# Performance work log

Hardware: AMD Instinct MI355X
Metric: run time of the kernel (lower is better)

Reference implementation:

```python
import jax, jax.numpy as jnp
import numpy as np

N_NODES = 50000
N_EDGES = 800000
N_REL = 2
K_SEL = 4096


def _glorot(key, shape):
    fan = shape[-2] + shape[-1]
    lim = jnp.sqrt(6.0 / fan)
    return jax.random.uniform(key, shape, minval=-lim, maxval=lim, dtype=jnp.float32)


def setup_inputs() -> dict:
    key = jax.random.key(0)
    ks = jax.random.split(key, 12)
    x = jax.random.normal(ks[0], (N_NODES, 128), jnp.float32)
    edge_index = jax.random.randint(ks[1], (2, N_EDGES), 0, N_NODES)
    edge_type = jax.random.randint(ks[2], (N_EDGES,), 0, N_REL)
    idx = jax.random.randint(ks[3], (K_SEL,), 0, N_NODES)
    # RGATConv 0: in=128, out=128, heads=2, dim=1 -> concat width 256
    w0 = _glorot(ks[4], (N_REL, 128, 256))
    q0 = _glorot(ks[5], (256, 2))
    k0 = _glorot(ks[6], (256, 2))
    b0 = jnp.zeros((256,), jnp.float32)
    g0 = jnp.ones((256,), jnp.float32)
    be0 = jnp.zeros((256,), jnp.float32)
    # RGATConv 1: in=256, out=128, heads=1
    w1 = _glorot(ks[7], (N_REL, 256, 128))
    q1 = _glorot(ks[8], (128, 1))
    k1 = _glorot(ks[9], (128, 1))
    b1 = jnp.zeros((128,), jnp.float32)
    g1 = jnp.ones((128,), jnp.float32)
    be1 = jnp.zeros((128,), jnp.float32)
    wm = _glorot(ks[10], (128, 5))
    bm = jnp.zeros((5,), jnp.float32)
    return dict(x=x, edge_index=edge_index, edge_type=edge_type, idx=idx,
                w0=w0, q0=q0, k0=k0, b0=b0, g0=g0, be0=be0,
                w1=w1, q1=q1, k1=k1, b1=b1, g1=g1, be1=be1, wm=wm, bm=bm)


def _segment_softmax(a, index, num_segments):
    # PyG utils.softmax: per-target max-shifted exp, normalized with +1e-16
    m = jax.ops.segment_max(a, index, num_segments=num_segments)
    m = jnp.where(jnp.isfinite(m), m, 0.0)
    e = jnp.exp(a - m[index])
    s = jax.ops.segment_sum(e, index, num_segments=num_segments)
    return e / (s[index] + 1e-16)


def _rgat(x, W, q, k, b, src, dst, edge_type, heads, out_ch, n):
    # additive-self-attention, across-relation, dim=1, aggr='add' (PyG defaults)
    xw = jnp.einsum('ni,rio->rno', x, W)          # [R, N, H*O]
    out_i = xw[edge_type, dst]                    # [E, H*O] gathered per edge
    out_j = xw[edge_type, src]                    # [E, H*O]
    alpha = jax.nn.leaky_relu(out_i @ q + out_j @ k, 0.2)   # [E, H]
    alpha = _segment_softmax(alpha, dst, n)
    msg = (alpha[:, :, None] * out_j.reshape(-1, heads, out_ch)).reshape(-1, heads * out_ch)
    return jax.ops.segment_sum(msg, dst, num_segments=n) + b


def _bn(h, g, b):
    # training-mode BatchNorm over nodes (biased var, eps=1e-5)
    mu = jnp.mean(h, axis=0)
    var = jnp.var(h, axis=0)
    return g * (h - mu) * jax.lax.rsqrt(var + 1e-5) + b


def reference(x, edge_index, edge_type, idx, w0, q0, k0, b0, g0, be0,
              w1, q1, k1, b1, g1, be1, wm, bm):
    n = x.shape[0]
    src, dst = edge_index[0], edge_index[1]
    h = jax.nn.leaky_relu(_rgat(x, w0, q0, k0, b0, src, dst, edge_type, 2, 128, n), 0.01)
    h = _bn(h, g0, be0)
    h = jax.nn.leaky_relu(_rgat(h, w1, q1, k1, b1, src, dst, edge_type, 1, 128, n), 0.01)
    h = _bn(h, g1, be1)
    h = h[idx]                                   # index_select over nodes
    out = jax.nn.sigmoid(h @ wm + bm)
    return (h, out)
```

## Files before the change

kernel.cpp:

```cpp
#include <hip/hip_runtime.h>
#include <hip/hip_bf16.h>
#include <math.h>


#define WAVE 64

typedef short     s16x8 __attribute__((ext_vector_type(8)));
typedef float     f32x4 __attribute__((ext_vector_type(4)));
typedef _Float16  f16x8 __attribute__((ext_vector_type(8)));
typedef _Float16  f16x4 __attribute__((ext_vector_type(4)));
typedef _Float16  f16x2 __attribute__((ext_vector_type(2)));

__device__ inline ushort bf_rne(float x) {
  uint u = __float_as_uint(x);
  return (ushort)((u + 0x7FFFu + ((u >> 16) & 1u)) >> 16);
}
__device__ inline ushort bf_hi_resid(float x, float& resid) {
  uint u = __float_as_uint(x);
  uint r = (u + 0x7FFFu + ((u >> 16) & 1u)) & 0xFFFF0000u;
  resid = x - __uint_as_float(r);
  return (ushort)(r >> 16);
}

__global__ __launch_bounds__(256) void k_hist(const int* __restrict__ dst,
                                              int* __restrict__ deg, int E) {
  int e = blockIdx.x * blockDim.x + threadIdx.x;
  if (e < E) atomicAdd(&deg[dst[e]], 1);
}

__global__ __launch_bounds__(256) void k_scan_blk(const int* __restrict__ deg,
                                                  int* __restrict__ bsum, int n) {
  int i = blockIdx.x * 256 + threadIdx.x;
  int v = (i < n) ? deg[i] : 0;
#pragma unroll
  for (int o = 32; o; o >>= 1) v += __shfl_xor(v, o);
  __shared__ int ws[4];
  if ((threadIdx.x & 63) == 0) ws[threadIdx.x >> 6] = v;
  __syncthreads();
  if (threadIdx.x == 0) bsum[blockIdx.x] = ws[0] + ws[1] + ws[2] + ws[3];
}

__global__ __launch_bounds__(256) void k_scan_top(int* __restrict__ bsum, int nb,
                                                  int* __restrict__ rowptr_n,
                                                  int E) {
  __shared__ int sh[256];
  int t = threadIdx.x;
  int carry = 0;
  for (int base = 0; base < nb; base += 256) {
    int i = base + t;
    int v = (i < nb) ? bsum[i] : 0;
    sh[t] = v;
    __syncthreads();
    for (int o = 1; o < 256; o <<= 1) {
      int u = (t >= o) ? sh[t - o] : 0;
      __syncthreads();
      sh[t] += u;
      __syncthreads();
    }
    if (i < nb) bsum[i] = carry + sh[t] - v;
    int blockTotal = sh[255];
    __syncthreads();
    carry += blockTotal;
  }
  if (t == 0) *rowptr_n = E;
}

__global__ __launch_bounds__(256) void k_scan_fin(const int* __restrict__ deg,
                                                  const int* __restrict__ bsum,
                                                  int* __restrict__ rowptr,
                                                  int* __restrict__ cursor, int n) {
  int t = threadIdx.x;
  int i = blockIdx.x * 256 + t;
  int v = (i < n) ? deg[i] : 0;
  __shared__ int sh[256];
  sh[t] = v;
  __syncthreads();
  for (int o = 1; o < 256; o <<= 1) {
    int u = (t >= o) ? sh[t - o] : 0;
    __syncthreads();
    sh[t] += u;
    __syncthreads();
  }
  if (i < n) {
    int ex = bsum[blockIdx.x] + sh[t] - v;
    rowptr[i] = ex;
    cursor[i] = ex;
  }
}

__global__ __launch_bounds__(256) void k_scatter(const int* __restrict__ dst,
                                                 int* __restrict__ cursor,
                                                 int* __restrict__ csr, int E) {
  int e = blockIdx.x * blockDim.x + threadIdx.x;
  if (e < E) {
    int p = atomicAdd(&cursor[dst[e]], 1);
    csr[p] = e;
  }
}

__global__ __launch_bounds__(256) void k_split(const float* __restrict__ in,
                                               ushort* __restrict__ hi,
                                               ushort* __restrict__ lo,
                                               const float* __restrict__ scale,
                                               const float* __restrict__ shift,
                                               int n4, int Cmask) {
  int i = blockIdx.x * blockDim.x + threadIdx.x;
  if (i >= n4) return;
  float4 v = ((const float4*)in)[i];
  if (scale) {
    int c = (i * 4) & Cmask;
    v.x = v.x * scale[c + 0] + shift[c + 0];
    v.y = v.y * scale[c + 1] + shift[c + 1];
    v.z = v.z * scale[c + 2] + shift[c + 2];
    v.w = v.w * scale[c + 3] + shift[c + 3];
  }
  float r0, r1, r2, r3;
  ushort4 hv, lv;
  hv.x = bf_hi_resid(v.x, r0); lv.x = bf_rne(r0);
  hv.y = bf_hi_resid(v.y, r1); lv.y = bf_rne(r1);
  hv.z = bf_hi_resid(v.z, r2); lv.z = bf_rne(r2);
  hv.w = bf_hi_resid(v.w, r3); lv.w = bf_rne(r3);
  ((ushort4*)hi)[i] = hv;
  ((ushort4*)lo)[i] = lv;
}

__global__ __launch_bounds__(256) void k_convW(const float* __restrict__ w,
                                               ushort* __restrict__ thi,
                                               ushort* __restrict__ tlo,
                                               int R, int K, int N) {
  int i = blockIdx.x * blockDim.x + threadIdx.x;
  if (i >= R * K * N) return;
  int n  = i % N;
  int t  = i / N;
  int kk = t % K;
  int r  = t / K;
  float x = w[i];
  float resid;
  ushort h = bf_hi_resid(x, resid);
  size_t o = ((size_t)r * N + n) * K + kk;
  thi[o] = h;
  tlo[o] = bf_rne(resid);
}

__global__ __launch_bounds__(256) void k_gemm_mfma(
    const ushort* __restrict__ Ahi, const ushort* __restrict__ Alo,
    const ushort* __restrict__ Bhi, const ushort* __restrict__ Blo,
    _Float16* __restrict__ C, int M, int K, int N) {
  const int r  = blockIdx.z;
  const int n0 = blockIdx.x * 128;
  const int m0 = blockIdx.y * 128;
  __shared__ __align__(16) ushort Ah[128][40];
  __shared__ __align__(16) ushort Al[128][40];
  __shared__ __align__(16) ushort Bh[128][40];
  __shared__ __align__(16) ushort Bl[128][40];
  const int tid  = threadIdx.x;
  const int lane = tid & 63;
  const int wid  = tid >> 6;
  const int wr = wid >> 1, wc = wid & 1;
  const int lr = lane & 15;
  const int lk = (lane >> 4) * 8;
  const size_t bbase = (size_t)r * N * K;

  f32x4 acc[4][4];
#pragma unroll
  for (int i = 0; i < 4; ++i)
#pragma unroll
    for (int j = 0; j < 4; ++j) acc[i][j] = (f32x4){0.f, 0.f, 0.f, 0.f};

  for (int k0 = 0; k0 < K; k0 += 32) {
#pragma unroll
    for (int rep = 0; rep < 2; ++rep) {
      int idx = tid + rep * 256;
      int row = idx >> 2, piece = idx & 3;
      int gm = m0 + row;
      s16x8 vh = (s16x8)0, vl = (s16x8)0;
      if (gm < M) {
        size_t ga = (size_t)gm * K + k0 + piece * 8;
        vh = *(const s16x8*)(Ahi + ga);
        vl = *(const s16x8*)(Alo + ga);
      }
      *(s16x8*)&Ah[row][piece * 8] = vh;
      *(s16x8*)&Al[row][piece * 8] = vl;
    }
#pragma unroll
    for (int rep = 0; rep < 2; ++rep) {
      int idx = tid + rep * 256;
      int col = idx >> 2, piece = idx & 3;
      size_t ga = bbase + (size_t)(n0 + col) * K + k0 + piece * 8;
      *(s16x8*)&Bh[col][piece * 8] = *(const s16x8*)(Bhi + ga);
      *(s16x8*)&Bl[col][piece * 8] = *(const s16x8*)(Blo + ga);
    }
    __syncthreads();

    s16x8 ah[4], al[4], bh[4], bl[4];
#pragma unroll
    for (int f = 0; f < 4; ++f) {
      ah[f] = *(const s16x8*)&Ah[wr * 64 + f * 16 + lr][lk];
      al[f] = *(const s16x8*)&Al[wr * 64 + f * 16 + lr][lk];
      bh[f] = *(const s16x8*)&Bh[wc * 64 + f * 16 + lr][lk];
      bl[f] = *(const s16x8*)&Bl[wc * 64 + f * 16 + lr][lk];
    }
#pragma unroll
    for (int fi = 0; fi < 4; ++fi)
#pragma unroll
      for (int fj = 0; fj < 4; ++fj) {
        acc[fi][fj] = __builtin_amdgcn_mfma_f32_16x16x32_bf16(
            ah[fi], bh[fj], acc[fi][fj], 0, 0, 0);
        acc[fi][fj] = __builtin_amdgcn_mfma_f32_16x16x32_bf16(
            ah[fi], bl[fj], acc[fi][fj], 0, 0, 0);
        acc[fi][fj] = __builtin_amdgcn_mfma_f32_16x16x32_bf16(
            al[fi], bh[fj], acc[fi][fj], 0, 0, 0);
      }
    __syncthreads();
  }

  _Float16* Cr = C + (size_t)r * M * N;
#pragma unroll
  for (int fi = 0; fi < 4; ++fi) {
#pragma unroll
    for (int v = 0; v < 4; ++v) {
      int row = m0 + wr * 64 + fi * 16 + (lane >> 4) * 4 + v;
      if (row < M) {
        size_t rb = (size_t)row * N + n0 + wc * 64 + lr;
#pragma unroll
        for (int fj = 0; fj < 4; ++fj)
          Cr[rb + fj * 16] = (_Float16)acc[fi][fj][v];
      }
    }
  }
}

template <int C, int H>
__global__ __launch_bounds__(256) void k_logits(const _Float16* __restrict__ xw,
                                                const float* __restrict__ qm,
                                                const float* __restrict__ km,
                                                float* __restrict__ ai,
                                                float* __restrict__ aj,
                                                int totalRows) {
  int g = blockIdx.x * blockDim.x + threadIdx.x;
  int row = g >> 2, q4 = g & 3;
  if (row >= totalRows) return;
  constexpr int QC = C / 4;
  const _Float16* rp = xw + (size_t)row * C + q4 * QC;
  float pq[H] = {}, pk[H] = {};
  for (int b = 0; b < QC; b += 8) {
    f16x8 v = *(const f16x8*)(rp + b);
#pragma unroll
    for (int e = 0; e < 8; ++e) {
      float f = (float)v[e];
      int c = q4 * QC + b + e;
#pragma unroll
      for (int h = 0; h < H; ++h) {
        pq[h] += f * qm[c * H + h];
        pk[h] += f * km[c * H + h];
      }
    }
  }
#pragma unroll
  for (int h = 0; h < H; ++h) {
    pq[h] += __shfl_xor(pq[h], 1); pq[h] += __shfl_xor(pq[h], 2);
    pk[h] += __shfl_xor(pk[h], 1); pk[h] += __shfl_xor(pk[h], 2);
  }
  if (q4 == 0) {
#pragma unroll
    for (int h = 0; h < H; ++h) {
      ai[(size_t)row * H + h] = pq[h];
      aj[(size_t)row * H + h] = pk[h];
    }
  }
}

template <int C, int H>
__global__ __launch_bounds__(256) void k_agg(const int* __restrict__ rowptr,
                                             const int* __restrict__ csr,
                                             const int* __restrict__ srcIdx,
                                             const int* __restrict__ etype,
                                             const float* __restrict__ ai,
                                             const float* __restrict__ aj,
                                             const _Float16* __restrict__ xw,
                                             const float* __restrict__ bias,
                                             float* __restrict__ out, int nNodes) {
  constexpr int VEC = C / WAVE;
  constexpr int OC  = C / H;
  int wid  = (blockIdx.x * blockDim.x + threadIdx.x) >> 6;
  int lane = threadIdx.x & 63;
  if (wid >= nNodes) return;
  const int node  = wid;
  const int start = rowptr[node];
  const int end   = rowptr[node + 1];
  const int deg   = end - start;
  const int myhead = (lane * VEC) / OC;

  float aiv[2][H];
#pragma unroll
  for (int rr = 0; rr < 2; ++rr)
#pragma unroll
    for (int h = 0; h < H; ++h)
      aiv[rr][h] = ai[((size_t)rr * nNodes + node) * H + h];

  float acc[VEC] = {};
  float ssum[H] = {};
  float m[H];

  if (deg <= WAVE) {
    int i = start + lane;
    bool valid = i < end;
    int e = valid ? csr[i] : 0;
    int s = valid ? srcIdx[e] : 0;
    int t = valid ? etype[e] : 0;
    float a[H], eh[H];
#pragma unroll
    for (int h = 0; h < H; ++h) {
      float v = aiv[t][h] + aj[((size_t)t * nNodes + s) * H + h];
      v = v > 0.f ? v : 0.2f * v;
      a[h] = valid ? v : -1e30f;
      m[h] = a[h];
    }
#pragma unroll
    for (int h = 0; h < H; ++h)
#pragma unroll
      for (int o = 32; o; o >>= 1) m[h] = fmaxf(m[h], __shfl_xor(m[h], o));
#pragma unroll
    for (int h = 0; h < H; ++h) {
      eh[h] = valid ? expf(a[h] - m[h]) : 0.f;
      ssum[h] = eh[h];
    }
#pragma unroll 4
    for (int j = 0; j < deg; ++j) {
      int   sj = __shfl(s, j);
      int   tj = __shfl(t, j);
      float c0 = __shfl(eh[0], j);
      float coef;
      if (H == 1) coef = c0;
      else { float c1 = __shfl(eh[H - 1], j); coef = myhead ? c1 : c0; }
      const _Float16* row = xw + ((size_t)tj * nNodes + sj) * C + lane * VEC;
      if constexpr (VEC == 4) {
        f16x4 rv = *(const f16x4*)row;
        acc[0] += coef * (float)rv[0]; acc[1] += coef * (float)rv[1];
        acc[2] += coef * (float)rv[2]; acc[3] += coef * (float)rv[3];
      } else {
        f16x2 rv = *(const f16x2*)row;
        acc[0] += coef * (float)rv[0]; acc[1] += coef * (float)rv[1];
      }
    }
  } else {
#pragma unroll
    for (int h = 0; h < H; ++h) m[h] = -1e30f;
    for (int i = start + lane; i < end; i += WAVE) {
      int e = csr[i];
      int s = srcIdx[e];
      int t = etype[e];
#pragma unroll
      for (int h = 0; h < H; ++h) {
        float v = aiv[t][h] + aj[((size_t)t * nNodes + s) * H + h];
        v = v > 0.f ? v : 0.2f * v;
        m[h] = fmaxf(m[h], v);
      }
    }
#pragma unroll
    for (int h = 0; h < H; ++h)
#pragma unroll
      for (int o = 32; o; o >>= 1) m[h] = fmaxf(m[h], __shfl_xor(m[h], o));

    for (int base = start; base < end; base += WAVE) {
      int i = base + lane;
      bool valid = i < end;
      int e = valid ? csr[i] : 0;
      int s = valid ? srcIdx[e] : 0;
      int t = valid ? etype[e] : 0;
      float eh[H];
#pragma unroll
      for (int h = 0; h < H; ++h) {
        float v = aiv[t][h] + aj[((size_t)t * nNodes + s) * H + h];
        v = v > 0.f ? v : 0.2f * v;
        eh[h] = valid ? expf(v - m[h]) : 0.f;
        ssum[h] += eh[h];
      }
      int cnt = end - base; if (cnt > WAVE) cnt = WAVE;
#pragma unroll 4
      for (int j = 0; j < cnt; ++j) {
        int   sj = __shfl(s, j);
        int   tj = __shfl(t, j);
        float c0 = __shfl(eh[0], j);
        float coef;
        if (H == 1) coef = c0;
        else { float c1 = __shfl(eh[H - 1], j); coef = myhead ? c1 : c0; }
        const _Float16* row = xw + ((size_t)tj * nNodes + sj) * C + lane * VEC;
        if constexpr (VEC == 4) {
          f16x4 rv = *(const f16x4*)row;
          acc[0] += coef * (float)rv[0]; acc[1] += coef * (float)rv[1];
          acc[2] += coef * (float)rv[2]; acc[3] += coef * (float)rv[3];
        } else {
          f16x2 rv = *(const f16x2*)row;
          acc[0] += coef * (float)rv[0]; acc[1] += coef * (float)rv[1];
        }
      }
    }
  }

#pragma unroll
  for (int h = 0; h < H; ++h)
#pragma unroll
    for (int o = 32; o; o >>= 1) ssum[h] += __shfl_xor(ssum[h], o);
  float inv = 1.f / (ssum[myhead] + 1e-16f);

#pragma unroll
  for (int v = 0; v < VEC; ++v) {
    int c = lane * VEC + v;
    float xo = acc[v] * inv + bias[c];
    out[(size_t)node * C + c] = xo > 0.f ? xo : 0.01f * xo;
  }
}

__global__ void k_bn_stats(const float* __restrict__ h, double* __restrict__ sum,
                           double* __restrict__ sumsq, int nNodes, int C) {
  int col = threadIdx.x;
  int r0 = blockIdx.x * 256;
  int r1 = r0 + 256; if (r1 > nNodes) r1 = nNodes;
  double s = 0.0, s2 = 0.0;
  for (int r = r0; r < r1; ++r) {
    float v = h[(size_t)r * C + col];
    s += v;
    s2 += (double)v * (double)v;
  }
  atomicAdd(&sum[col], s);
  atomicAdd(&sumsq[col], s2);
}

__global__ void k_bn_finalize(const double* __restrict__ sum,
                              const double* __restrict__ sumsq,
                              const float* __restrict__ g,
                              const float* __restrict__ be,
                              float* __restrict__ scale,
                              float* __restrict__ shift, int nNodes, int C) {
  int c = blockIdx.x * blockDim.x + threadIdx.x;
  if (c >= C) return;
  double mu  = sum[c] / nNodes;
  double var = sumsq[c] / nNodes - mu * mu;
  float rs = (float)(1.0 / sqrt(var + 1e-5));
  float sc = g[c] * rs;
  scale[c] = sc;
  shift[c] = be[c] - (float)mu * sc;
}

__global__ __launch_bounds__(256) void k_head(const float* __restrict__ h,
                                              const int* __restrict__ idx,
                                              const float* __restrict__ scl,
                                              const float* __restrict__ shf,
                                              const float* __restrict__ wm,
                                              const float* __restrict__ bm,
                                              float* __restrict__ outH,
                                              float* __restrict__ outP, int kSel) {
  int wid  = (blockIdx.x * blockDim.x + threadIdx.x) >> 6;
  int lane = threadIdx.x & 63;
  if (wid >= kSel) return;
  int node = idx[wid];
  const float* row = h + (size_t)node * 128;
  int c = lane * 2;
  float2 v = *(const float2*)&row[c];
  v.x = v.x * scl[c + 0] + shf[c + 0];
  v.y = v.y * scl[c + 1] + shf[c + 1];
  *(float2*)&outH[(size_t)wid * 128 + c] = v;
  float p0 = v.x * wm[c * 5 + 0] + v.y * wm[(c + 1) * 5 + 0];
  float p1 = v.x * wm[c * 5 + 1] + v.y * wm[(c + 1) * 5 + 1];
  float p2 = v.x * wm[c * 5 + 2] + v.y * wm[(c + 1) * 5 + 2];
  float p3 = v.x * wm[c * 5 + 3] + v.y * wm[(c + 1) * 5 + 3];
  float p4 = v.x * wm[c * 5 + 4] + v.y * wm[(c + 1) * 5 + 4];
#pragma unroll
  for (int o = 32; o; o >>= 1) {
    p0 += __shfl_xor(p0, o); p1 += __shfl_xor(p1, o); p2 += __shfl_xor(p2, o);
    p3 += __shfl_xor(p3, o); p4 += __shfl_xor(p4, o);
  }
  if (lane == 0) {
    float lg[5] = {p0 + bm[0], p1 + bm[1], p2 + bm[2], p3 + bm[3], p4 + bm[4]};
    float* o = &outP[(size_t)wid * 5];
    o[0] = 1.f / (1.f + expf(-lg[0]));
    o[1] = 1.f / (1.f + expf(-lg[1]));
    o[2] = 1.f / (1.f + expf(-lg[2]));
    o[3] = 1.f / (1.f + expf(-lg[3]));
    o[4] = 1.f / (1.f + expf(-lg[4]));
  }
}

extern "C" void kernel_launch(void* const* d_in, const int* in_sizes, int n_in,
                              void* d_out, int out_size, void* d_ws, size_t ws_size,
                              hipStream_t stream) {
  const float* x    = (const float*)d_in[0];
  const int*   ei   = (const int*)d_in[1];
  const int*   etyp = (const int*)d_in[2];
  const int*   idx  = (const int*)d_in[3];
  const float* w0   = (const float*)d_in[4];
  const float* q0   = (const float*)d_in[5];
  const float* k0   = (const float*)d_in[6];
  const float* b0   = (const float*)d_in[7];
  const float* g0   = (const float*)d_in[8];
  const float* be0  = (const float*)d_in[9];
  const float* w1   = (const float*)d_in[10];
  const float* q1   = (const float*)d_in[11];
  const float* k1   = (const float*)d_in[12];
  const float* b1   = (const float*)d_in[13];
  const float* g1   = (const float*)d_in[14];
  const float* be1  = (const float*)d_in[15];
  const float* wm   = (const float*)d_in[16];
  const float* bm   = (const float*)d_in[17];

  const int N    = in_sizes[0] / 128;
  const int E    = in_sizes[1] / 2;
  const int kSel = in_sizes[3];
  const int* srcIdx = ei;
  const int* dstIdx = ei + E;

  size_t off = 0;
  auto carve = [&](size_t bytes) -> void* {
    off = (off + 255) & ~(size_t)255;
    void* p = (char*)d_ws + off;
    off += bytes;
    return p;
  };
  int*      deg    = (int*)carve((size_t)N * 4);
  int*      rowptr = (int*)carve((size_t)(N + 1) * 4);
  int*      cursor = (int*)carve((size_t)N * 4);
  int*      bsum   = (int*)carve((size_t)((N + 255) / 256) * 4);
  int*      csr    = (int*)carve((size_t)E * 4);
  _Float16* xwh    = (_Float16*)carve((size_t)2 * N * 256 * 2);
  ushort*   Ahi    = (ushort*)carve((size_t)N * 256 * 2);
  ushort*   Alo    = (ushort*)carve((size_t)N * 256 * 2);
  ushort*   W0thi  = (ushort*)carve((size_t)2 * 256 * 128 * 2);
  ushort*   W0tlo  = (ushort*)carve((size_t)2 * 256 * 128 * 2);
  ushort*   W1thi  = (ushort*)carve((size_t)2 * 256 * 128 * 2);
  ushort*   W1tlo  = (ushort*)carve((size_t)2 * 256 * 128 * 2);
  float*    ai     = (float*)carve((size_t)2 * N * 2 * 4);
  float*    aj     = (float*)carve((size_t)2 * N * 2 * 4);
  float*    h0     = (float*)carve((size_t)N * 256 * 4);
  float*    h1     = (float*)carve((size_t)N * 128 * 4);
  double*   dsum   = (double*)carve(256 * 8);
  double*   dsumsq = (double*)carve(256 * 8);
  float*    scl    = (float*)carve(256 * 4);
  float*    shf    = (float*)carve(256 * 4);

  float* outH = (float*)d_out;
  float* outP = outH + (size_t)kSel * 128;

  const int eb = (E + 255) / 256;
  const int nbBlocks = (N + 255) / 256;

  hipMemsetAsync(deg, 0, (size_t)N * 4, stream);
  k_hist<<<eb, 256, 0, stream>>>(dstIdx, deg, E);
  k_scan_blk<<<nbBlocks, 256, 0, stream>>>(deg, bsum, N);
  k_scan_top<<<1, 256, 0, stream>>>(bsum, nbBlocks, rowptr + N, E);
  k_scan_fin<<<nbBlocks, 256, 0, stream>>>(deg, bsum, rowptr, cursor, N);
  k_scatter<<<eb, 256, 0, stream>>>(dstIdx, cursor, csr, E);

  k_convW<<<(2 * 128 * 256 + 255) / 256, 256, 0, stream>>>(w0, W0thi, W0tlo,
                                                           2, 128, 256);
  k_convW<<<(2 * 256 * 128 + 255) / 256, 256, 0, stream>>>(w1, W1thi, W1tlo,
                                                           2, 256, 128);

  k_split<<<((N * 128 / 4) + 255) / 256, 256, 0, stream>>>(
      x, Ahi, Alo, nullptr, nullptr, N * 128 / 4, 0);
  {
    dim3 grid(256 / 128, (N + 127) / 128, 2);
    k_gemm_mfma<<<grid, 256, 0, stream>>>(Ahi, Alo, W0thi, W0tlo, xwh,
                                          N, 128, 256);
  }
  k_logits<256, 2><<<(2 * N * 4 + 255) / 256, 256, 0, stream>>>(
      xwh, q0, k0, ai, aj, 2 * N);
  k_agg<256, 2><<<(N * WAVE + 255) / 256, 256, 0, stream>>>(
      rowptr, csr, srcIdx, etyp, ai, aj, xwh, b0, h0, N);
  hipMemsetAsync(dsum, 0, 256 * 8, stream);
  hipMemsetAsync(dsumsq, 0, 256 * 8, stream);
  k_bn_stats<<<(N + 255) / 256, 256, 0, stream>>>(h0, dsum, dsumsq, N, 256);
  k_bn_finalize<<<1, 256, 0, stream>>>(dsum, dsumsq, g0, be0, scl, shf, N, 256);

  k_split<<<((N * 256 / 4) + 255) / 256, 256, 0, stream>>>(
      h0, Ahi, Alo, scl, shf, N * 256 / 4, 255);
  {
    dim3 grid(128 / 128, (N + 127) / 128, 2);
    k_gemm_mfma<<<grid, 256, 0, stream>>>(Ahi, Alo, W1thi, W1tlo, xwh,
                                          N, 256, 128);
  }
  k_logits<128, 1><<<(2 * N * 4 + 255) / 256, 256, 0, stream>>>(
      xwh, q1, k1, ai, aj, 2 * N);
  k_agg<128, 1><<<(N * WAVE + 255) / 256, 256, 0, stream>>>(
      rowptr, csr, srcIdx, etyp, ai, aj, xwh, b1, h1, N);
  hipMemsetAsync(dsum, 0, 128 * 8, stream);
  hipMemsetAsync(dsumsq, 0, 128 * 8, stream);
  k_bn_stats<<<(N + 255) / 256, 128, 0, stream>>>(h1, dsum, dsumsq, N, 128);
  k_bn_finalize<<<1, 128, 0, stream>>>(dsum, dsumsq, g1, be1, scl, shf, N, 128);

  k_head<<<(kSel * WAVE + 255) / 256, 256, 0, stream>>>(
      h1, idx, scl, shf, wm, bm, outH, outP, kSel);
}
```

Baseline: 680.3 us.

## Fold BatchNorm into layer-1 weights and fuse bf16 split into aggregation

Layer-0 aggregation now writes the hi/lo bf16 split directly instead of an fp32 buffer, which removes the separate split pass and the fp32 h0 round trip. BatchNorm scale is folded into W1 during conversion, and the shift becomes a per-column bias added in the GEMM epilogue. The aggregation kernel for low-degree nodes processes several edges per wave with 8-wide fp16 loads and cross-lane reduction. BN stats accumulate per thread in float before the double atomics, which adds some rounding in exchange for cheaper arithmetic.

```diff
diff --git a/kernel.cpp b/kernel.cpp
--- a/kernel.cpp
+++ b/kernel.cpp
@@ -6,10 +6,9 @@
 #define WAVE 64
 
 typedef short     s16x8 __attribute__((ext_vector_type(8)));
+typedef ushort    u16x8 __attribute__((ext_vector_type(8)));
 typedef float     f32x4 __attribute__((ext_vector_type(4)));
 typedef _Float16  f16x8 __attribute__((ext_vector_type(8)));
-typedef _Float16  f16x4 __attribute__((ext_vector_type(4)));
-typedef _Float16  f16x2 __attribute__((ext_vector_type(2)));
 
 __device__ inline ushort bf_rne(float x) {
   uint u = __float_as_uint(x);
@@ -20,6 +19,9 @@
   uint r = (u + 0x7FFFu + ((u >> 16) & 1u)) & 0xFFFF0000u;
   resid = x - __uint_as_float(r);
   return (ushort)(r >> 16);
+}
+__device__ inline float bf2f(ushort h) {
+  return __uint_as_float(((uint)h) << 16);
 }
 
 __global__ __launch_bounds__(256) void k_hist(const int* __restrict__ dst,
@@ -100,20 +102,10 @@
 
 __global__ __launch_bounds__(256) void k_split(const float* __restrict__ in,
                                                ushort* __restrict__ hi,
-                                               ushort* __restrict__ lo,
-                                               const float* __restrict__ scale,
-                                               const float* __restrict__ shift,
-                                               int n4, int Cmask) {
+                                               ushort* __restrict__ lo, int n4) {
   int i = blockIdx.x * blockDim.x + threadIdx.x;
   if (i >= n4) return;
   float4 v = ((const float4*)in)[i];
-  if (scale) {
-    int c = (i * 4) & Cmask;
-    v.x = v.x * scale[c + 0] + shift[c + 0];
-    v.y = v.y * scale[c + 1] + shift[c + 1];
-    v.z = v.z * scale[c + 2] + shift[c + 2];
-    v.w = v.w * scale[c + 3] + shift[c + 3];
-  }
   float r0, r1, r2, r3;
   ushort4 hv, lv;
   hv.x = bf_hi_resid(v.x, r0); lv.x = bf_rne(r0);
@@ -127,6 +119,7 @@
 __global__ __launch_bounds__(256) void k_convW(const float* __restrict__ w,
                                                ushort* __restrict__ thi,
                                                ushort* __restrict__ tlo,
+                                               const float* __restrict__ scale,
                                                int R, int K, int N) {
   int i = blockIdx.x * blockDim.x + threadIdx.x;
   if (i >= R * K * N) return;
@@ -135,6 +128,7 @@
   int kk = t % K;
   int r  = t / K;
   float x = w[i];
+  if (scale) x *= scale[kk];
   float resid;
   ushort h = bf_hi_resid(x, resid);
   size_t o = ((size_t)r * N + n) * K + kk;
@@ -142,10 +136,24 @@
   tlo[o] = bf_rne(resid);
 }
 
+__global__ __launch_bounds__(256) void k_biasW(const float* __restrict__ w,
+                                               const float* __restrict__ shf,
+                                               float* __restrict__ cbias,
+                                               int R, int K, int N) {
+  int t = blockIdx.x * blockDim.x + threadIdx.x;
+  if (t >= R * N) return;
+  int n = t % N, r = t / N;
+  float s = 0.f;
+  for (int k = 0; k < K; ++k)
+    s += shf[k] * w[((size_t)r * K + k) * N + n];
+  cbias[t] = s;
+}
+
 __global__ __launch_bounds__(256) void k_gemm_mfma(
     const ushort* __restrict__ Ahi, const ushort* __restrict__ Alo,
     const ushort* __restrict__ Bhi, const ushort* __restrict__ Blo,
-    _Float16* __restrict__ C, int M, int K, int N) {
+    const float* __restrict__ cbias, _Float16* __restrict__ C,
+    int M, int K, int N) {
   const int r  = blockIdx.z;
   const int n0 = blockIdx.x * 128;
   const int m0 = blockIdx.y * 128;
@@ -214,6 +222,12 @@
     __syncthreads();
   }
 
+  float bz[4] = {0.f, 0.f, 0.f, 0.f};
+  if (cbias) {
+#pragma unroll
+    for (int fj = 0; fj < 4; ++fj)
+      bz[fj] = cbias[r * N + n0 + wc * 64 + fj * 16 + lr];
+  }
   _Float16* Cr = C + (size_t)r * M * N;
 #pragma unroll
   for (int fi = 0; fi < 4; ++fi) {
@@ -224,7 +238,7 @@
         size_t rb = (size_t)row * N + n0 + wc * 64 + lr;
 #pragma unroll
         for (int fj = 0; fj < 4; ++fj)
-          Cr[rb + fj * 16] = (_Float16)acc[fi][fj][v];
+          Cr[rb + fj * 16] = (_Float16)(acc[fi][fj][v] + bz[fj]);
       }
     }
   }
@@ -270,7 +284,7 @@
   }
 }
 
-template <int C, int H>
+template <int C, int H, bool SPLIT>
 __global__ __launch_bounds__(256) void k_agg(const int* __restrict__ rowptr,
                                              const int* __restrict__ csr,
                                              const int* __restrict__ srcIdx,
@@ -279,8 +293,12 @@
                                              const float* __restrict__ aj,
                                              const _Float16* __restrict__ xw,
                                              const float* __restrict__ bias,
-                                             float* __restrict__ out, int nNodes) {
-  constexpr int VEC = C / WAVE;
+                                             float* __restrict__ out32,
+                                             ushort* __restrict__ ohi,
+                                             ushort* __restrict__ olo,
+                                             int nNodes) {
+  constexpr int LPE = C / 8;
+  constexpr int EPW = WAVE / LPE;
   constexpr int OC  = C / H;
   int wid  = (blockIdx.x * blockDim.x + threadIdx.x) >> 6;
   int lane = threadIdx.x & 63;
@@ -289,7 +307,6 @@
   const int start = rowptr[node];
   const int end   = rowptr[node + 1];
   const int deg   = end - start;
-  const int myhead = (lane * VEC) / OC;
 
   float aiv[2][H];
 #pragma unroll
@@ -297,10 +314,6 @@
 #pragma unroll
     for (int h = 0; h < H; ++h)
       aiv[rr][h] = ai[((size_t)rr * nNodes + node) * H + h];
-
-  float acc[VEC] = {};
-  float ssum[H] = {};
-  float m[H];
 
   if (deg <= WAVE) {
     int i = start + lane;
@@ -308,7 +321,7 @@
     int e = valid ? csr[i] : 0;
     int s = valid ? srcIdx[e] : 0;
     int t = valid ? etype[e] : 0;
-    float a[H], eh[H];
+    float a[H], eh[H], m[H], ssum[H];
 #pragma unroll
     for (int h = 0; h < H; ++h) {
       float v = aiv[t][h] + aj[((size_t)t * nNodes + s) * H + h];
@@ -324,26 +337,65 @@
     for (int h = 0; h < H; ++h) {
       eh[h] = valid ? expf(a[h] - m[h]) : 0.f;
       ssum[h] = eh[h];
-    }
-#pragma unroll 4
-    for (int j = 0; j < deg; ++j) {
-      int   sj = __shfl(s, j);
-      int   tj = __shfl(t, j);
-      float c0 = __shfl(eh[0], j);
+#pragma unroll
+      for (int o = 32; o; o >>= 1) ssum[h] += __shfl_xor(ssum[h], o);
+    }
+
+    const int sub = lane / LPE;
+    const int cl  = lane % LPE;
+    const int c0  = cl * 8;
+    const int myhead = c0 / OC;
+
+    float acc[8] = {};
+#pragma unroll 2
+    for (int j = 0; j < deg; j += EPW) {
+      int je = j + sub;
+      int   sj = __shfl(s, je);
+      int   tj = __shfl(t, je);
+      float cc0 = __shfl(eh[0], je);
       float coef;
-      if (H == 1) coef = c0;
-      else { float c1 = __shfl(eh[H - 1], j); coef = myhead ? c1 : c0; }
-      const _Float16* row = xw + ((size_t)tj * nNodes + sj) * C + lane * VEC;
-      if constexpr (VEC == 4) {
-        f16x4 rv = *(const f16x4*)row;
-        acc[0] += coef * (float)rv[0]; acc[1] += coef * (float)rv[1];
-        acc[2] += coef * (float)rv[2]; acc[3] += coef * (float)rv[3];
+      if (H == 1) coef = cc0;
+      else { float cc1 = __shfl(eh[H - 1], je); coef = myhead ? cc1 : cc0; }
+      f16x8 rv = *(const f16x8*)(xw + ((size_t)tj * nNodes + sj) * C + c0);
+#pragma unroll
+      for (int v = 0; v < 8; ++v) acc[v] += coef * (float)rv[v];
+    }
+#pragma unroll
+    for (int v = 0; v < 8; ++v) {
+      if (EPW == 4) acc[v] += __shfl_xor(acc[v], 16);
+      acc[v] += __shfl_xor(acc[v], 32);
+    }
+    float inv = 1.f / (ssum[myhead] + 1e-16f);
+    if (sub == 0) {
+      if constexpr (SPLIT) {
+        u16x8 hv, lv;
+#pragma unroll
+        for (int v = 0; v < 8; ++v) {
+          float xo = acc[v] * inv + bias[c0 + v];
+          xo = xo > 0.f ? xo : 0.01f * xo;
+          float resid;
+          hv[v] = bf_hi_resid(xo, resid);
+          lv[v] = bf_rne(resid);
+        }
+        *(u16x8*)&ohi[(size_t)node * C + c0] = hv;
+        *(u16x8*)&olo[(size_t)node * C + c0] = lv;
       } else {
-        f16x2 rv = *(const f16x2*)row;
-        acc[0] += coef * (float)rv[0]; acc[1] += coef * (float)rv[1];
+        float ov[8];
+#pragma unroll
+        for (int v = 0; v < 8; ++v) {
+          float xo = acc[v] * inv + bias[c0 + v];
+          ov[v] = xo > 0.f ? xo : 0.01f * xo;
+        }
+        *(float4*)&out32[(size_t)node * C + c0]     = *(float4*)&ov[0];
+        *(float4*)&out32[(size_t)node * C + c0 + 4] = *(float4*)&ov[4];
       }
     }
   } else {
+    constexpr int VEC = C / WAVE;
+    const int myhead = (lane * VEC) / OC;
+    float acc[VEC] = {};
+    float ssum[H] = {};
+    float m[H];
 #pragma unroll
     for (int h = 0; h < H; ++h) m[h] = -1e30f;
     for (int i = start + lane; i < end; i += WAVE) {
@@ -361,7 +413,6 @@
     for (int h = 0; h < H; ++h)
 #pragma unroll
       for (int o = 32; o; o >>= 1) m[h] = fmaxf(m[h], __shfl_xor(m[h], o));
-
     for (int base = start; base < end; base += WAVE) {
       int i = base + lane;
       bool valid = i < end;
@@ -381,34 +432,33 @@
       for (int j = 0; j < cnt; ++j) {
         int   sj = __shfl(s, j);
         int   tj = __shfl(t, j);
-        float c0 = __shfl(eh[0], j);
+        float cc0 = __shfl(eh[0], j);
         float coef;
-        if (H == 1) coef = c0;
-        else { float c1 = __shfl(eh[H - 1], j); coef = myhead ? c1 : c0; }
+        if (H == 1) coef = cc0;
+        else { float cc1 = __shfl(eh[H - 1], j); coef = myhead ? cc1 : cc0; }
         const _Float16* row = xw + ((size_t)tj * nNodes + sj) * C + lane * VEC;
-        if constexpr (VEC == 4) {
-          f16x4 rv = *(const f16x4*)row;
-          acc[0] += coef * (float)rv[0]; acc[1] += coef * (float)rv[1];
-          acc[2] += coef * (float)rv[2]; acc[3] += coef * (float)rv[3];
-        } else {
-          f16x2 rv = *(const f16x2*)row;
-          acc[0] += coef * (float)rv[0]; acc[1] += coef * (float)rv[1];
-        }
-      }
-    }
-  }
-
-#pragma unroll
-  for (int h = 0; h < H; ++h)
-#pragma unroll
-    for (int o = 32; o; o >>= 1) ssum[h] += __shfl_xor(ssum[h], o);
-  float inv = 1.f / (ssum[myhead] + 1e-16f);
-
-#pragma unroll
-  for (int v = 0; v < VEC; ++v) {
-    int c = lane * VEC + v;
-    float xo = acc[v] * inv + bias[c];
-    out[(size_t)node * C + c] = xo > 0.f ? xo : 0.01f * xo;
+#pragma unroll
+        for (int v = 0; v < VEC; ++v) acc[v] += coef * (float)row[v];
+      }
+    }
+#pragma unroll
+    for (int h = 0; h < H; ++h)
+#pragma unroll
+      for (int o = 32; o; o >>= 1) ssum[h] += __shfl_xor(ssum[h], o);
+    float inv = 1.f / (ssum[myhead] + 1e-16f);
+#pragma unroll
+    for (int v = 0; v < VEC; ++v) {
+      int c = lane * VEC + v;
+      float xo = acc[v] * inv + bias[c];
+      xo = xo > 0.f ? xo : 0.01f * xo;
+      if constexpr (SPLIT) {
+        float resid;
+        ohi[(size_t)node * C + c] = bf_hi_resid(xo, resid);
+        olo[(size_t)node * C + c] = bf_rne(resid);
+      } else {
+        out32[(size_t)node * C + c] = xo;
+      }
+    }
   }
 }
 
@@ -417,14 +467,32 @@
   int col = threadIdx.x;
   int r0 = blockIdx.x * 256;
   int r1 = r0 + 256; if (r1 > nNodes) r1 = nNodes;
-  double s = 0.0, s2 = 0.0;
+  float s = 0.f, s2 = 0.f;
   for (int r = r0; r < r1; ++r) {
     float v = h[(size_t)r * C + col];
     s += v;
-    s2 += (double)v * (double)v;
-  }
-  atomicAdd(&sum[col], s);
-  atomicAdd(&sumsq[col], s2);
+    s2 = fmaf(v, v, s2);
+  }
+  atomicAdd(&sum[col], (double)s);
+  atomicAdd(&sumsq[col], (double)s2);
+}
+
+__global__ void k_bn_stats_hl(const ushort* __restrict__ hi,
+                              const ushort* __restrict__ lo,
+                              double* __restrict__ sum,
+                              double* __restrict__ sumsq, int nNodes, int C) {
+  int col = threadIdx.x;
+  int r0 = blockIdx.x * 256;
+  int r1 = r0 + 256; if (r1 > nNodes) r1 = nNodes;
+  float s = 0.f, s2 = 0.f;
+  for (int r = r0; r < r1; ++r) {
+    size_t o = (size_t)r * C + col;
+    float v = bf2f(hi[o]) + bf2f(lo[o]);
+    s += v;
+    s2 = fmaf(v, v, s2);
+  }
+  atomicAdd(&sum[col], (double)s);
+  atomicAdd(&sumsq[col], (double)s2);
 }
 
 __global__ void k_bn_finalize(const double* __restrict__ sum,
@@ -529,9 +597,9 @@
   ushort*   W0tlo  = (ushort*)carve((size_t)2 * 256 * 128 * 2);
   ushort*   W1thi  = (ushort*)carve((size_t)2 * 256 * 128 * 2);
   ushort*   W1tlo  = (ushort*)carve((size_t)2 * 256 * 128 * 2);
+  float*    cbias1 = (float*)carve(256 * 4);
   float*    ai     = (float*)carve((size_t)2 * N * 2 * 4);
   float*    aj     = (float*)carve((size_t)2 * N * 2 * 4);
-  float*    h0     = (float*)carve((size_t)N * 256 * 4);
   float*    h1     = (float*)carve((size_t)N * 128 * 4);
   double*   dsum   = (double*)carve(256 * 8);
   double*   dsumsq = (double*)carve(256 * 8);
@@ -551,41 +619,41 @@
   k_scan_fin<<<nbBlocks, 256, 0, stream>>>(deg, bsum, rowptr, cursor, N);
   k_scatter<<<eb, 256, 0, stream>>>(dstIdx, cursor, csr, E);
 
-  k_convW<<<(2 * 128 * 256 + 255) / 256, 256, 0, stream>>>(w0, W0thi, W0tlo,
-                                                           2, 128, 256);
-  k_convW<<<(2 * 256 * 128 + 255) / 256, 256, 0, stream>>>(w1, W1thi, W1tlo,
-                                                           2, 256, 128);
-
+  k_convW<<<(2 * 128 * 256 + 255) / 256, 256, 0, stream>>>(
+      w0, W0thi, W0tlo, nullptr, 2, 128, 256);
   k_split<<<((N * 128 / 4) + 255) / 256, 256, 0, stream>>>(
-      x, Ahi, Alo, nullptr, nullptr, N * 128 / 4, 0);
+      x, Ahi, Alo, N * 128 / 4);
+
   {
     dim3 grid(256 / 128, (N + 127) / 128, 2);
-    k_gemm_mfma<<<grid, 256, 0, stream>>>(Ahi, Alo, W0thi, W0tlo, xwh,
-                                          N, 128, 256);
+    k_gemm_mfma<<<grid, 256, 0, stream>>>(Ahi, Alo, W0thi, W0tlo, nullptr,
+                                          xwh, N, 128, 256);
   }
   k_logits<256, 2><<<(2 * N * 4 + 255) / 256, 256, 0, stream>>>(
       xwh, q0, k0, ai, aj, 2 * N);
-  k_agg<256, 2><<<(N * WAVE + 255) / 256, 256, 0, stream>>>(
-      rowptr, csr, srcIdx, etyp, ai, aj, xwh, b0, h0, N);
+  k_agg<256, 2, true><<<(N * WAVE + 255) / 256, 256, 0, stream>>>(
+      rowptr, csr, srcIdx, etyp, ai, aj, xwh, b0, nullptr, Ahi, Alo, N);
   hipMemsetAsync(dsum, 0, 256 * 8, stream);
   hipMemsetAsync(dsumsq, 0, 256 * 8, stream);
-  k_bn_stats<<<(N + 255) / 256, 256, 0, stream>>>(h0, dsum, dsumsq, N, 256);
+  k_bn_stats_hl<<<nbBlocks, 256, 0, stream>>>(Ahi, Alo, dsum, dsumsq, N, 256);
   k_bn_finalize<<<1, 256, 0, stream>>>(dsum, dsumsq, g0, be0, scl, shf, N, 256);
 
-  k_split<<<((N * 256 / 4) + 255) / 256, 256, 0, stream>>>(
-      h0, Ahi, Alo, scl, shf, N * 256 / 4, 255);
+  k_convW<<<(2 * 256 * 128 + 255) / 256, 256, 0, stream>>>(
+      w1, W1thi, W1tlo, scl, 2, 256, 128);
+  k_biasW<<<1, 256, 0, stream>>>(w1, shf, cbias1, 2, 256, 128);
+
   {
     dim3 grid(128 / 128, (N + 127) / 128, 2);
-    k_gemm_mfma<<<grid, 256, 0, stream>>>(Ahi, Alo, W1thi, W1tlo, xwh,
-                                          N, 256, 128);
+    k_gemm_mfma<<<grid, 256, 0, stream>>>(Ahi, Alo, W1thi, W1tlo, cbias1,
+                                          xwh, N, 256, 128);
   }
   k_logits<128, 1><<<(2 * N * 4 + 255) / 256, 256, 0, stream>>>(
       xwh, q1, k1, ai, aj, 2 * N);
-  k_agg<128, 1><<<(N * WAVE + 255) / 256, 256, 0, stream>>>(
-      rowptr, csr, srcIdx, etyp, ai, aj, xwh, b1, h1, N);
+  k_agg<128, 1, false><<<(N * WAVE + 255) / 256, 256, 0, stream>>>(
+      rowptr, csr, srcIdx, etyp, ai, aj, xwh, b1, h1, nullptr, nullptr, N);
   hipMemsetAsync(dsum, 0, 128 * 8, stream);
   hipMemsetAsync(dsumsq, 0, 128 * 8, stream);
-  k_bn_stats<<<(N + 255) / 256, 128, 0, stream>>>(h1, dsum, dsumsq, N, 128);
+  k_bn_stats<<<nbBlocks, 128, 0, stream>>>(h1, dsum, dsumsq, N, 128);
   k_bn_finalize<<<1, 128, 0, stream>>>(dsum, dsumsq, g1, be1, scl, shf, N, 128);
 
   k_head<<<(kSel * WAVE + 255) / 256, 256, 0, stream>>>(
```

Result: slower. 716.8 us (+5.4%).
